# Performance work log

Hardware: AMD Instinct MI355X
Metric: run time of the kernel (lower is better)

Reference implementation:

```python
import jax, jax.numpy as jnp
import numpy as np

DIM = 768
HEADS = 6
LEVELS = 3
POINTS = 4
HID = int(DIM * 0.25)  # 192
B = 4
H0 = 64
W0 = 64
NQ = H0 * W0
SHAPES = [(128, 128), (64, 64), (32, 32)]
NV = sum(h * w for h, w in SHAPES)
EPS = 1e-6


def _ln(x, g, b):
    m = x.mean(-1, keepdims=True)
    v = ((x - m) ** 2).mean(-1, keepdims=True)
    return (x - m) / jnp.sqrt(v + EPS) * g + b


def _bilinear(img, grid, Hl, Wl):
    # img: [BH, Hl*Wl, d], grid: [BH, Np, 2] in [-1,1] (x=width, y=height)
    # grid_sample semantics: bilinear, padding zeros, align_corners=False
    gx, gy = grid[..., 0], grid[..., 1]
    x = (gx + 1) * (Wl * 0.5) - 0.5
    y = (gy + 1) * (Hl * 0.5) - 0.5
    x0 = jnp.floor(x)
    y0 = jnp.floor(y)
    wx = x - x0
    wy = y - y0
    x0i = x0.astype(jnp.int32)
    y0i = y0.astype(jnp.int32)

    def corner(xi, yi, wgt):
        valid = (xi >= 0) & (xi < Wl) & (yi >= 0) & (yi < Hl)
        idx = jnp.clip(yi, 0, Hl - 1) * Wl + jnp.clip(xi, 0, Wl - 1)
        v = jnp.take_along_axis(img, idx[..., None], axis=1)
        return v * (wgt * valid)[..., None]

    return (corner(x0i, y0i, (1 - wx) * (1 - wy))
            + corner(x0i + 1, y0i, wx * (1 - wy))
            + corner(x0i, y0i + 1, (1 - wx) * wy)
            + corner(x0i + 1, y0i + 1, wx * wy))


def setup_inputs() -> dict:
    key = jax.random.key(0)
    ks = jax.random.split(key, 24)
    s = 0.02
    inp = {
        'query': jax.random.normal(ks[0], (B, NQ, DIM), jnp.float32),
        'reference_points': jax.random.uniform(ks[1], (B, NQ, LEVELS, 2), jnp.float32),
        'feat': jax.random.normal(ks[2], (B, NV, DIM), jnp.float32),
        'spatial_shapes': jnp.array(SHAPES, dtype=jnp.int32),
        'level_start_index': jnp.array(np.cumsum([0] + [h * w for h, w in SHAPES])[:-1], dtype=jnp.int32),
        'H': H0,
        'W': W0,
        'qn_g': jnp.ones((DIM,)), 'qn_b': jnp.zeros((DIM,)),
        'fn_g': jnp.ones((DIM,)), 'fn_b': jnp.zeros((DIM,)),
        'off_w': jax.random.normal(ks[3], (DIM, HEADS * LEVELS * POINTS * 2)) * s,
        'off_b': jax.random.normal(ks[4], (HEADS * LEVELS * POINTS * 2,)) * s,
        'aw_w': jax.random.normal(ks[5], (DIM, HEADS * LEVELS * POINTS)) * s,
        'aw_b': jnp.zeros((HEADS * LEVELS * POINTS,)),
        'vp_w': jax.random.normal(ks[6], (DIM, DIM)) * s,
        'vp_b': jnp.zeros((DIM,)),
        'op_w': jax.random.normal(ks[7], (DIM, DIM)) * s,
        'op_b': jnp.zeros((DIM,)),
        'ffn_g': jnp.ones((DIM,)), 'ffn_b': jnp.zeros((DIM,)),
        'fc1_w': jax.random.normal(ks[8], (DIM, HID)) * s,
        'fc1_b': jnp.zeros((HID,)),
        'dw_w': jax.random.normal(ks[9], (3, 3, 1, HID)) * s,
        'dw_b': jnp.zeros((HID,)),
        'fc2_w': jax.random.normal(ks[10], (HID, DIM)) * s,
        'fc2_b': jnp.zeros((DIM,)),
    }
    return inp


def reference(query, reference_points, feat, spatial_shapes, level_start_index, H, W,
              qn_g, qn_b, fn_g, fn_b, off_w, off_b, aw_w, aw_b, vp_w, vp_b, op_w, op_b,
              ffn_g, ffn_b, fc1_w, fc1_b, dw_w, dw_b, fc2_w, fc2_b):
    shapes = [(int(h), int(w)) for h, w in np.asarray(spatial_shapes)]
    starts = np.cumsum([0] + [h * w for h, w in shapes])[:-1]
    Bq, Nq, C = query.shape
    d = C // HEADS

    q = _ln(query, qn_g, qn_b)                       # query_norm
    v = _ln(feat, fn_g, fn_b) @ vp_w + vp_b          # feat_norm + value_proj
    v = v.reshape(Bq, -1, HEADS, d)

    off = (q @ off_w + off_b).reshape(Bq, Nq, HEADS, LEVELS, POINTS, 2)
    aw = (q @ aw_w + aw_b).reshape(Bq, Nq, HEADS, LEVELS * POINTS)
    aw = jax.nn.softmax(aw, axis=-1).reshape(Bq, Nq, HEADS, LEVELS, POINTS)

    # offset normalizer is (W, H) per level
    norm = jnp.array([[w_, h_] for h_, w_ in shapes], dtype=query.dtype)
    loc = reference_points[:, :, None, :, None, :] + off / norm[None, None, None, :, None, :]
    grids = 2.0 * loc - 1.0                          # [B,Nq,heads,L,P,2]

    outs = []
    for l, (hl, wl) in enumerate(shapes):
        vl = v[:, starts[l]:starts[l] + hl * wl]     # [B, hl*wl, heads, d]
        vl = vl.transpose(0, 2, 1, 3).reshape(Bq * HEADS, hl * wl, d)
        g = grids[:, :, :, l].transpose(0, 2, 1, 3, 4).reshape(Bq * HEADS, Nq * POINTS, 2)
        s = _bilinear(vl, g, hl, wl).reshape(Bq, HEADS, Nq, POINTS, d)
        outs.append(s)
    samp = jnp.stack(outs, axis=3)                   # [B,heads,Nq,L,P,d]
    w_att = aw.transpose(0, 2, 1, 3, 4)              # [B,heads,Nq,L,P]
    out = (samp * w_att[..., None]).sum(axis=(3, 4)) # [B,heads,Nq,d]
    out = out.transpose(0, 2, 1, 3).reshape(Bq, Nq, C)
    attn = out @ op_w + op_b + q                     # mmcv adds identity (=normed query)

    x = query + attn

    # ConvFFN: fc1 -> DWConv -> GELU -> fc2, residual
    y = _ln(x, ffn_g, ffn_b) @ fc1_w + fc1_b         # [B,Nq,HID]
    y2 = y.reshape(Bq, H, W, HID)
    y2 = jax.lax.conv_general_dilated(
        y2, dw_w, window_strides=(1, 1), padding='SAME',
        feature_group_count=HID,
        dimension_numbers=('NHWC', 'HWIO', 'NHWC')) + dw_b
    y = jax.nn.gelu(y2.reshape(Bq, Nq, HID), approximate=False)
    y = y @ fc2_w + fc2_b
    return x + y
```

## Files before the change

kernel.cpp:

```cpp
#include <hip/hip_runtime.h>
#include <hip/hip_bf16.h>

constexpr int kDIM = 768;
constexpr int kHEADS = 6;
constexpr int kLEVELS = 3;
constexpr int kPOINTS = 4;
constexpr int kHID = 192;
constexpr int kB = 4;
constexpr int kH0 = 64;
constexpr int kW0 = 64;
constexpr int kNQ = kH0 * kW0;
constexpr int kNV = 21504;
constexpr int kDH = 128;
constexpr float kEPS = 1e-6f;
constexpr int kOAW = 256;

typedef __attribute__((ext_vector_type(8))) short short8;
typedef __attribute__((ext_vector_type(4))) float floatx4;
typedef __attribute__((ext_vector_type(4))) unsigned int uintx4;

__device__ __forceinline__ float bf2f(__hip_bfloat16 x) { return __bfloat162float(x); }
__device__ __forceinline__ float bflo2f(unsigned int u) { return __uint_as_float(u << 16); }
__device__ __forceinline__ float bfhi2f(unsigned int u) { return __uint_as_float(u & 0xffff0000u); }
__device__ __forceinline__ unsigned short f2bfu(float f) {
  __hip_bfloat16 h = __float2bfloat16(f);
  return *reinterpret_cast<unsigned short*>(&h);
}

#define GLD_LDS16(g, l) \
  __builtin_amdgcn_global_load_lds( \
      (const __attribute__((address_space(1))) void*)(g), \
      (__attribute__((address_space(3))) void*)(l), 16, 0, 0)

__global__ __launch_bounds__(256) void ln_bf16_kernel(
    const float* __restrict__ x, const float* __restrict__ g,
    const float* __restrict__ b, __hip_bfloat16* __restrict__ out)
{
  constexpr int MT = 8;
  int tid = threadIdx.x, grp = tid >> 5, lane = tid & 31;
  size_t row = (size_t)blockIdx.x * MT + grp;
  const float* xr = x + row * kDIM;
  float buf[kDIM / 32];
  float s = 0.f;
#pragma unroll
  for (int i = 0; i < kDIM / 32; ++i) { float v = xr[lane + i * 32]; buf[i] = v; s += v; }
  for (int d = 16; d > 0; d >>= 1) s += __shfl_down(s, d, 32);
  float mean = __shfl(s, 0, 32) * (1.f / kDIM);
  float vs = 0.f;
#pragma unroll
  for (int i = 0; i < kDIM / 32; ++i) { float d = buf[i] - mean; vs += d * d; }
  for (int d = 16; d > 0; d >>= 1) vs += __shfl_down(vs, d, 32);
  float rstd = rsqrtf(__shfl(vs, 0, 32) * (1.f / kDIM) + kEPS);
  __hip_bfloat16* orow = out + row * kDIM;
#pragma unroll
  for (int i = 0; i < kDIM / 32; ++i) {
    int k = lane + i * 32;
    orow[k] = __float2bfloat16((buf[i] - mean) * rstd * g[k] + b[k]);
  }
}

__global__ __launch_bounds__(256) void transpose_w_kernel(
    const float* __restrict__ w, __hip_bfloat16* __restrict__ wt)
{
  int t = blockIdx.x * 256 + threadIdx.x;
  int n = t / kDIM, k = t % kDIM;
  wt[t] = __float2bfloat16(w[(size_t)k * kDIM + n]);
}

template <int K, int N, int NPAD>
__global__ __launch_bounds__(256) void prep_wt_kernel(
    const float* __restrict__ w, const float* __restrict__ b,
    __hip_bfloat16* __restrict__ wt, float* __restrict__ bp)
{
  int t = blockIdx.x * 256 + threadIdx.x;
  int n = t / K, k = t % K;
  float v = (n < N) ? w[(size_t)k * N + n] : 0.f;
  wt[t] = __float2bfloat16(v);
  if (bp != nullptr && t < NPAD) bp[t] = (t < N) ? b[t] : 0.f;
}

__global__ __launch_bounds__(256) void prep_offaw_w_kernel(
    const float* __restrict__ ow, const float* __restrict__ aww,
    const float* __restrict__ ob, const float* __restrict__ awb,
    __hip_bfloat16* __restrict__ wt, float* __restrict__ bias)
{
  int t = blockIdx.x * 256 + threadIdx.x;
  int n = t / kDIM, k = t % kDIM;
  float v = 0.f;
  if (n < 144)       v = ow[(size_t)k * 144 + n];
  else if (n < 216)  v = aww[(size_t)k * 72 + (n - 144)];
  wt[t] = __float2bfloat16(v);
  if (t < kOAW) {
    float b = 0.f;
    if (t < 144)       b = ob[t];
    else if (t < 216)  b = awb[t - 144];
    bias[t] = b;
  }
}

template <int EPI, int KK>
__global__ __launch_bounds__(256) void gemm_bt_kernel(
    const unsigned short* __restrict__ A, const unsigned short* __restrict__ Bt,
    const float* __restrict__ bias,
    __hip_bfloat16* __restrict__ outB,
    const __hip_bfloat16* __restrict__ qln, const float* __restrict__ query,
    float* __restrict__ outF)
{
  constexpr int K = KK;
  constexpr int LDC = (EPI == 2) ? kOAW : kDIM;
  __shared__ unsigned short sA[128 * 64];
  __shared__ unsigned short sB[128 * 64];
  int tid = threadIdx.x;
  int wave = tid >> 6, lane = tid & 63;
  int tm = blockIdx.y * 128, tn = blockIdx.x * 128;
  int wm = (wave & 1) * 64, wn = (wave >> 1) * 64;
  floatx4 acc[4][4] = {};

  int sm_ = lane >> 3;
  int sc_ = lane & 7;

  for (int k0 = 0; k0 < K; k0 += 64) {
    __syncthreads();
#pragma unroll
    for (int i = 0; i < 4; ++i) {
      int base_m = i * 32 + wave * 8;
      int m = base_m + sm_;
      int csrc = sc_ ^ (m & 7);
      GLD_LDS16(A + (size_t)(tm + m) * K + k0 + csrc * 8,
                (char*)sA + base_m * 128);
      GLD_LDS16(Bt + (size_t)(tn + m) * K + k0 + csrc * 8,
                (char*)sB + base_m * 128);
    }
    __syncthreads();
#pragma unroll
    for (int s = 0; s < 2; ++s) {
      int kc = s * 4 + (lane >> 4);
      short8 af[4], bfr[4];
#pragma unroll
      for (int i = 0; i < 4; ++i) {
        int mm = wm + i * 16 + (lane & 15);
        af[i] = *(const short8*)((const char*)sA + mm * 128 + ((kc ^ (mm & 7)) * 16));
        int nn = wn + i * 16 + (lane & 15);
        bfr[i] = *(const short8*)((const char*)sB + nn * 128 + ((kc ^ (nn & 7)) * 16));
      }
#pragma unroll
      for (int i = 0; i < 4; ++i)
#pragma unroll
        for (int j = 0; j < 4; ++j)
          acc[i][j] = __builtin_amdgcn_mfma_f32_16x16x32_bf16(af[i], bfr[j], acc[i][j], 0, 0, 0);
    }
  }

  int r0 = (lane >> 4) * 4, cc = lane & 15;
#pragma unroll
  for (int i = 0; i < 4; ++i) {
    int rowb = tm + wm + i * 16 + r0;
#pragma unroll
    for (int j = 0; j < 4; ++j) {
      int col = tn + wn + j * 16 + cc;
      float bv = bias[col];
#pragma unroll
      for (int r = 0; r < 4; ++r) {
        size_t o = (size_t)(rowb + r) * LDC + col;
        float val = acc[i][j][r] + bv;
        if constexpr (EPI == 0) {
          outB[o] = __float2bfloat16(val);
        } else if constexpr (EPI == 1) {
          outF[o] = val + bf2f(qln[o]) + query[o];
        } else if constexpr (EPI == 2) {
          outF[o] = val;
        } else {
          outF[o] = val + query[o];
        }
      }
    }
  }
}

__global__ __launch_bounds__(256) void aw_softmax_kernel(float* __restrict__ raw)
{
  int t = blockIdx.x * 256 + threadIdx.x;
  int row = t / kHEADS, h = t % kHEADS;
  float* p = raw + (size_t)row * kOAW + 144 + h * 12;
  float v[12];
  float m = -1e30f;
#pragma unroll
  for (int j = 0; j < 12; ++j) { v[j] = p[j]; m = fmaxf(m, v[j]); }
  float den = 0.f;
#pragma unroll
  for (int j = 0; j < 12; ++j) { v[j] = expf(v[j] - m); den += v[j]; }
  float inv = 1.f / den;
#pragma unroll
  for (int j = 0; j < 12; ++j) p[j] = v[j] * inv;
}

__global__ __launch_bounds__(192) void sample_kernel(
    const float* __restrict__ offaw,
    const float* __restrict__ refp, const __hip_bfloat16* __restrict__ v,
    __hip_bfloat16* __restrict__ samp)
{
  __shared__ __align__(16) int   idx_s[2][72][4];
  __shared__ __align__(16) float w_s[2][72][4];
  int tid = threadIdx.x;
  int bq0 = blockIdx.x * 2;

  if (tid < 144) {
    int q = (tid >= 72) ? 1 : 0;
    int t = tid - q * 72;
    int bq = bq0 + q;
    const int LH[3] = {128, 64, 32};
    const int LST[3] = {0, 16384, 20480};
    int h2 = t / 12, j = t % 12, l = j >> 2, p = j & 3;
    int Wl = LH[l];
    const float* base = offaw + (size_t)bq * kOAW;
    float rx = refp[(size_t)bq * 6 + l * 2 + 0];
    float ry = refp[(size_t)bq * 6 + l * 2 + 1];
    float ox = base[h2 * 24 + l * 8 + p * 2 + 0];
    float oy = base[h2 * 24 + l * 8 + p * 2 + 1];
    float wgt = base[144 + h2 * 12 + l * 4 + p];
    float xx = rx * Wl + ox - 0.5f;
    float yy = ry * Wl + oy - 0.5f;
    float x0f = floorf(xx), y0f = floorf(yy);
    int x0 = (int)x0f, y0 = (int)y0f;
    float wx = xx - x0f, wy = yy - y0f;
#pragma unroll
    for (int cy = 0; cy < 2; ++cy) {
#pragma unroll
      for (int cx = 0; cx < 2; ++cx) {
        int xi = x0 + cx, yi = y0 + cy;
        bool valid = (xi >= 0) && (xi < Wl) && (yi >= 0) && (yi < Wl);
        int xc = min(max(xi, 0), Wl - 1), yc = min(max(yi, 0), Wl - 1);
        float cw = (cx ? wx : 1.f - wx) * (cy ? wy : 1.f - wy);
        idx_s[q][t][cy * 2 + cx] = (LST[l] + yc * Wl + xc) * kDIM;
        w_s[q][t][cy * 2 + cx] = valid ? cw * wgt : 0.f;
      }
    }
  }
  __syncthreads();

  int q = (tid >= 96) ? 1 : 0;
  int t = tid - q * 96;
  int bq = bq0 + q;
  int b = bq >> 12;
  int h = t >> 4, c0 = (t & 15) * 8;
  const __hip_bfloat16* vb = v + (size_t)b * kNV * kDIM + h * kDH + c0;
  float a[8] = {};
#pragma unroll
  for (int j = 0; j < 12; ++j) {
    int tt = h * 12 + j;
    int4 ii = *(const int4*)idx_s[q][tt];
    float4 ww = *(const float4*)w_s[q][tt];
#pragma unroll
    for (int k = 0; k < 4; ++k) {
      int idx = (k == 0) ? ii.x : (k == 1) ? ii.y : (k == 2) ? ii.z : ii.w;
      float wv = (k == 0) ? ww.x : (k == 1) ? ww.y : (k == 2) ? ww.z : ww.w;
      uintx4 uv = *(const uintx4*)(vb + idx);
      a[0] += wv * bflo2f(uv.x); a[1] += wv * bfhi2f(uv.x);
      a[2] += wv * bflo2f(uv.y); a[3] += wv * bfhi2f(uv.y);
      a[4] += wv * bflo2f(uv.z); a[5] += wv * bfhi2f(uv.z);
      a[6] += wv * bflo2f(uv.w); a[7] += wv * bfhi2f(uv.w);
    }
  }
  uintx4 ov;
  ov.x = (unsigned)f2bfu(a[0]) | ((unsigned)f2bfu(a[1]) << 16);
  ov.y = (unsigned)f2bfu(a[2]) | ((unsigned)f2bfu(a[3]) << 16);
  ov.z = (unsigned)f2bfu(a[4]) | ((unsigned)f2bfu(a[5]) << 16);
  ov.w = (unsigned)f2bfu(a[6]) | ((unsigned)f2bfu(a[7]) << 16);
  *(uintx4*)(samp + (size_t)bq * kDIM + h * kDH + c0) = ov;
}

__global__ __launch_bounds__(256) void dwconv_gelu_kernel(
    const float* __restrict__ y1, const float* __restrict__ w,
    const float* __restrict__ bias, __hip_bfloat16* __restrict__ y2)
{
  int idx = blockIdx.x * 256 + threadIdx.x;
  int c = idx % kHID;
  int sp = idx / kHID;
  int j = sp % kW0;
  int i = (sp / kW0) % kH0;
  int b = sp / (kW0 * kH0);
  float s = bias[c];
#pragma unroll
  for (int ky = 0; ky < 3; ++ky) {
    int yi = i + ky - 1;
    if (yi < 0 || yi >= kH0) continue;
#pragma unroll
    for (int kx = 0; kx < 3; ++kx) {
      int xj = j + kx - 1;
      if (xj < 0 || xj >= kW0) continue;
      s += y1[(((size_t)b * kH0 + yi) * kW0 + xj) * kOAW + c] * w[(ky * 3 + kx) * kHID + c];
    }
  }
  float gl = 0.5f * s * (1.f + erff(s * 0.70710678118654752440f));
  y2[idx] = __float2bfloat16(gl);
}

extern "C" void kernel_launch(void* const* d_in, const int* in_sizes, int n_in,
                              void* d_out, int out_size, void* d_ws, size_t ws_size,
                              hipStream_t stream)
{
  const float* query = (const float*)d_in[0];
  const float* refp  = (const float*)d_in[1];
  const float* feat  = (const float*)d_in[2];
  const float* qn_g  = (const float*)d_in[7];
  const float* qn_b  = (const float*)d_in[8];
  const float* fn_g  = (const float*)d_in[9];
  const float* fn_b  = (const float*)d_in[10];
  const float* off_w = (const float*)d_in[11];
  const float* off_b = (const float*)d_in[12];
  const float* aw_w  = (const float*)d_in[13];
  const float* aw_b  = (const float*)d_in[14];
  const float* vp_w  = (const float*)d_in[15];
  const float* vp_b  = (const float*)d_in[16];
  const float* op_w  = (const float*)d_in[17];
  const float* op_b  = (const float*)d_in[18];
  const float* ffn_g = (const float*)d_in[19];
  const float* ffn_b = (const float*)d_in[20];
  const float* fc1_w = (const float*)d_in[21];
  const float* fc1_b = (const float*)d_in[22];
  const float* dw_w  = (const float*)d_in[23];
  const float* dw_b  = (const float*)d_in[24];
  const float* fc2_w = (const float*)d_in[25];
  const float* fc2_b = (const float*)d_in[26];

  char* ws = (char*)d_ws;
  constexpr size_t kWsNeeded = 218400768ull;
  if (ws_size < kWsNeeded) return;

  __hip_bfloat16* a_ln     = (__hip_bfloat16*)(ws + 0);
  __hip_bfloat16* q_ln     = (__hip_bfloat16*)(ws + 0);
  __hip_bfloat16* x_ln     = (__hip_bfloat16*)(ws + 0);
  float*          y1p      = (float*)(ws + 25165824ull);
  __hip_bfloat16* samp     = (__hip_bfloat16*)(ws + 39321600ull);
  __hip_bfloat16* y2       = (__hip_bfloat16*)(ws + 41943040ull);
  __hip_bfloat16* v        = (__hip_bfloat16*)(ws + 66060288ull);
  float*          x        = (float*)(ws + 66060288ull);
  __hip_bfloat16* vp_w_t   = (__hip_bfloat16*)(ws + 198180864ull);
  __hip_bfloat16* op_w_t   = (__hip_bfloat16*)(ws + 199360512ull);
  float*          oa_raw   = (float*)(ws + 200540160ull);
  __hip_bfloat16* oa_wt    = (__hip_bfloat16*)(ws + 217317376ull);
  float*          oa_bias  = (float*)(ws + 217710592ull);
  __hip_bfloat16* fc1_wt   = (__hip_bfloat16*)(ws + 217711616ull);
  float*          fc1_bp   = (float*)(ws + 218104832ull);
  __hip_bfloat16* fc2_wt   = (__hip_bfloat16*)(ws + 218105856ull);

  constexpr int NROWQ = kB * kNQ;
  constexpr int NROWV = kB * kNV;
  constexpr int CHUNK = NROWV / 2;

  transpose_w_kernel<<<(kDIM * kDIM) / 256, 256, 0, stream>>>(vp_w, vp_w_t);
  transpose_w_kernel<<<(kDIM * kDIM) / 256, 256, 0, stream>>>(op_w, op_w_t);
  prep_offaw_w_kernel<<<(kOAW * kDIM) / 256, 256, 0, stream>>>(
      off_w, aw_w, off_b, aw_b, oa_wt, oa_bias);
  prep_wt_kernel<768, 192, 256><<<(256 * 768) / 256, 256, 0, stream>>>(
      fc1_w, fc1_b, fc1_wt, fc1_bp);
  prep_wt_kernel<192, 768, 768><<<(768 * 192) / 256, 256, 0, stream>>>(
      fc2_w, nullptr, fc2_wt, nullptr);

  for (int c = 0; c < 2; ++c) {
    ln_bf16_kernel<<<CHUNK / 8, 256, 0, stream>>>(
        feat + (size_t)c * CHUNK * kDIM, fn_g, fn_b, a_ln);
    gemm_bt_kernel<0, kDIM><<<dim3(kDIM / 128, CHUNK / 128), 256, 0, stream>>>(
        (const unsigned short*)a_ln, (const unsigned short*)vp_w_t, vp_b,
        v + (size_t)c * CHUNK * kDIM, nullptr, nullptr, nullptr);
  }

  ln_bf16_kernel<<<NROWQ / 8, 256, 0, stream>>>(query, qn_g, qn_b, q_ln);
  gemm_bt_kernel<2, kDIM><<<dim3(kOAW / 128, NROWQ / 128), 256, 0, stream>>>(
      (const unsigned short*)q_ln, (const unsigned short*)oa_wt, oa_bias,
      nullptr, nullptr, nullptr, oa_raw);
  aw_softmax_kernel<<<(NROWQ * kHEADS) / 256, 256, 0, stream>>>(oa_raw);
  sample_kernel<<<NROWQ / 2, 192, 0, stream>>>(oa_raw, refp, v, samp);
  gemm_bt_kernel<1, kDIM><<<dim3(kDIM / 128, NROWQ / 128), 256, 0, stream>>>(
      (const unsigned short*)samp, (const unsigned short*)op_w_t, op_b,
      nullptr, q_ln, query, x);

  ln_bf16_kernel<<<NROWQ / 8, 256, 0, stream>>>(x, ffn_g, ffn_b, x_ln);
  gemm_bt_kernel<2, kDIM><<<dim3(kOAW / 128, NROWQ / 128), 256, 0, stream>>>(
      (const unsigned short*)x_ln, (const unsigned short*)fc1_wt, fc1_bp,
      nullptr, nullptr, nullptr, y1p);
  dwconv_gelu_kernel<<<(NROWQ * kHID) / 256, 256, 0, stream>>>(y1p, dw_w, dw_b, y2);
  gemm_bt_kernel<3, kHID><<<dim3(kDIM / 128, NROWQ / 128), 256, 0, stream>>>(
      (const unsigned short*)y2, (const unsigned short*)fc2_wt, fc2_b,
      nullptr, nullptr, x, (float*)d_out);
}
```

Baseline: 869.7 us.

## Add 256x256 double-buffered GEMM for value projection and vectorize LayerNorm

Replaces the 128x128 single-stage GEMM used for the large value projection (86k rows) with a 256x256 tile, 512-thread kernel that double-buffers LDS via global_load_lds, swizzles LDS columns, remaps block order for L2 locality and raises MFMA wave priority. Separately, the LayerNorm kernel now uses float4 loads and ushort4 stores. The larger tile is meant to cut redundant global traffic and hide load latency, at the cost of 128KB LDS per block and higher register pressure that may limit occupancy. The grid is 2*84*3 blocks per chunk, which may leave a tail.

Result: faster. 835.1 us (-4.0%).

```diff
diff --git a/kernel.cpp b/kernel.cpp
--- a/kernel.cpp
+++ b/kernel.cpp
@@ -37,25 +37,42 @@
     const float* __restrict__ b, __hip_bfloat16* __restrict__ out)
 {
   constexpr int MT = 8;
+  constexpr int NV4 = kDIM / 4 / 32;
   int tid = threadIdx.x, grp = tid >> 5, lane = tid & 31;
   size_t row = (size_t)blockIdx.x * MT + grp;
-  const float* xr = x + row * kDIM;
-  float buf[kDIM / 32];
+  const float4* xr = (const float4*)(x + row * kDIM);
+  float4 buf[NV4];
   float s = 0.f;
 #pragma unroll
-  for (int i = 0; i < kDIM / 32; ++i) { float v = xr[lane + i * 32]; buf[i] = v; s += v; }
+  for (int i = 0; i < NV4; ++i) {
+    float4 v = xr[lane + i * 32];
+    buf[i] = v;
+    s += v.x + v.y + v.z + v.w;
+  }
   for (int d = 16; d > 0; d >>= 1) s += __shfl_down(s, d, 32);
   float mean = __shfl(s, 0, 32) * (1.f / kDIM);
   float vs = 0.f;
 #pragma unroll
-  for (int i = 0; i < kDIM / 32; ++i) { float d = buf[i] - mean; vs += d * d; }
+  for (int i = 0; i < NV4; ++i) {
+    float4 v = buf[i];
+    float d0 = v.x - mean, d1 = v.y - mean, d2 = v.z - mean, d3 = v.w - mean;
+    vs += d0 * d0 + d1 * d1 + d2 * d2 + d3 * d3;
+  }
   for (int d = 16; d > 0; d >>= 1) vs += __shfl_down(vs, d, 32);
   float rstd = rsqrtf(__shfl(vs, 0, 32) * (1.f / kDIM) + kEPS);
-  __hip_bfloat16* orow = out + row * kDIM;
-#pragma unroll
-  for (int i = 0; i < kDIM / 32; ++i) {
+  const float4* gg = (const float4*)g;
+  const float4* bb = (const float4*)b;
+  ushort4* orow = (ushort4*)(out + row * kDIM);
+#pragma unroll
+  for (int i = 0; i < NV4; ++i) {
     int k = lane + i * 32;
-    orow[k] = __float2bfloat16((buf[i] - mean) * rstd * g[k] + b[k]);
+    float4 gv = gg[k], bv = bb[k], v = buf[i];
+    ushort4 o;
+    o.x = f2bfu((v.x - mean) * rstd * gv.x + bv.x);
+    o.y = f2bfu((v.y - mean) * rstd * gv.y + bv.y);
+    o.z = f2bfu((v.z - mean) * rstd * gv.z + bv.z);
+    o.w = f2bfu((v.w - mean) * rstd * gv.w + bv.w);
+    orow[k] = o;
   }
 }
 
@@ -98,6 +115,87 @@
   }
 }
 
+__global__ __launch_bounds__(512, 2) void gemm256_bt_kernel(
+    const unsigned short* __restrict__ A, const unsigned short* __restrict__ Bt,
+    const float* __restrict__ bias, __hip_bfloat16* __restrict__ outB, int nx)
+{
+  constexpr int K = kDIM;
+  __shared__ unsigned short sA[2][256 * 64];
+  __shared__ unsigned short sB[2][256 * 64];
+  int tid = threadIdx.x;
+  int wave = tid >> 6, lane = tid & 63;
+
+  int cpx = gridDim.x >> 3;
+  int orig = blockIdx.x;
+  int swz = (orig & 7) * cpx + (orig >> 3);
+  int tn = (swz % nx) * 256;
+  int tm = (swz / nx) * 256;
+
+  int wmb = (wave >> 2) * 128;
+  int wnb = (wave & 3) * 64;
+  floatx4 acc[8][4] = {};
+  int sr = lane >> 3, sc = lane & 7;
+
+  auto stage = [&](unsigned short* dA, unsigned short* dB, int k0) {
+#pragma unroll
+    for (int i = 0; i < 4; ++i) {
+      int base = i * 64 + wave * 8;
+      int m = base + sr;
+      int cs = sc ^ (m & 7);
+      GLD_LDS16(A + (size_t)(tm + m) * K + k0 + cs * 8, (char*)dA + base * 128);
+      GLD_LDS16(Bt + (size_t)(tn + m) * K + k0 + cs * 8, (char*)dB + base * 128);
+    }
+  };
+
+  stage(sA[0], sB[0], 0);
+  __syncthreads();
+
+  for (int t = 0; t < K / 64; ++t) {
+    int cur = t & 1;
+    if (t < K / 64 - 1) stage(sA[cur ^ 1], sB[cur ^ 1], (t + 1) * 64);
+    const char* pA = (const char*)sA[cur];
+    const char* pB = (const char*)sB[cur];
+#pragma unroll
+    for (int kk = 0; kk < 2; ++kk) {
+      int kc = kk * 4 + (lane >> 4);
+      short8 af[8], bfr[4];
+#pragma unroll
+      for (int i = 0; i < 8; ++i) {
+        int mm = wmb + i * 16 + (lane & 15);
+        af[i] = *(const short8*)(pA + mm * 128 + ((kc ^ (mm & 7)) * 16));
+      }
+#pragma unroll
+      for (int j = 0; j < 4; ++j) {
+        int nn = wnb + j * 16 + (lane & 15);
+        bfr[j] = *(const short8*)(pB + nn * 128 + ((kc ^ (nn & 7)) * 16));
+      }
+      __builtin_amdgcn_s_setprio(1);
+#pragma unroll
+      for (int i = 0; i < 8; ++i)
+#pragma unroll
+        for (int j = 0; j < 4; ++j)
+          acc[i][j] = __builtin_amdgcn_mfma_f32_16x16x32_bf16(af[i], bfr[j], acc[i][j], 0, 0, 0);
+      __builtin_amdgcn_s_setprio(0);
+      if (kk == 0) __builtin_amdgcn_s_barrier();
+    }
+    __syncthreads();
+  }
+
+  int r0 = (lane >> 4) * 4, cc = lane & 15;
+#pragma unroll
+  for (int i = 0; i < 8; ++i) {
+    int rowb = tm + wmb + i * 16 + r0;
+#pragma unroll
+    for (int j = 0; j < 4; ++j) {
+      int col = tn + wnb + j * 16 + cc;
+      float bv = bias[col];
+#pragma unroll
+      for (int r = 0; r < 4; ++r)
+        outB[(size_t)(rowb + r) * kDIM + col] = __float2bfloat16(acc[i][j][r] + bv);
+    }
+  }
+}
+
 template <int EPI, int KK>
 __global__ __launch_bounds__(256) void gemm_bt_kernel(
     const unsigned short* __restrict__ A, const unsigned short* __restrict__ Bt,
@@ -163,9 +261,7 @@
       for (int r = 0; r < 4; ++r) {
         size_t o = (size_t)(rowb + r) * LDC + col;
         float val = acc[i][j][r] + bv;
-        if constexpr (EPI == 0) {
-          outB[o] = __float2bfloat16(val);
-        } else if constexpr (EPI == 1) {
+        if constexpr (EPI == 1) {
           outF[o] = val + bf2f(qln[o]) + query[o];
         } else if constexpr (EPI == 2) {
           outF[o] = val;
@@ -360,9 +456,9 @@
   for (int c = 0; c < 2; ++c) {
     ln_bf16_kernel<<<CHUNK / 8, 256, 0, stream>>>(
         feat + (size_t)c * CHUNK * kDIM, fn_g, fn_b, a_ln);
-    gemm_bt_kernel<0, kDIM><<<dim3(kDIM / 128, CHUNK / 128), 256, 0, stream>>>(
+    gemm256_bt_kernel<<<(CHUNK / 256) * (kDIM / 256), 512, 0, stream>>>(
         (const unsigned short*)a_ln, (const unsigned short*)vp_w_t, vp_b,
-        v + (size_t)c * CHUNK * kDIM, nullptr, nullptr, nullptr);
+        v + (size_t)c * CHUNK * kDIM, kDIM / 256);
   }
 
   ln_bf16_kernel<<<NROWQ / 8, 256, 0, stream>>>(query, qn_g, qn_b, q_ln);
```
